# Performance work log

Hardware: AMD Instinct MI355X
Metric: run time of the kernel (lower is better)

Reference implementation:

```python
import jax, jax.numpy as jnp
import numpy as np

N, C, K = 200000, 128, 27  # active voxels, channels, 3x3x3 kernel taps
EPS = 1e-5  # torch LayerNorm default


def setup_inputs() -> dict:
    key = jax.random.key(0)
    ks = jax.random.split(key, 8)
    feats = jax.random.normal(ks[0], (N, C), dtype=jnp.float32)
    # plan-based gather map: neighbor row index per voxel per kernel tap
    neighbor_idx = jax.random.randint(ks[1], (N, K), 0, N, dtype=jnp.int32)
    # sparse conv weights: one [C_in, C_out] slice per kernel offset
    conv_w = jax.random.normal(ks[2], (K, C, C), dtype=jnp.float32) * (1.0 / np.sqrt(K * C))
    conv_b = jax.random.normal(ks[3], (C,), dtype=jnp.float32) * 0.02
    # torch.nn.Linear(C, C): weight [out, in], y = x @ W^T + b
    lin_w = jax.random.normal(ks[4], (C, C), dtype=jnp.float32) * (1.0 / np.sqrt(C))
    lin_b = jax.random.normal(ks[5], (C,), dtype=jnp.float32) * 0.02
    ln_w = 1.0 + 0.02 * jax.random.normal(ks[6], (C,), dtype=jnp.float32)
    ln_b = 0.02 * jax.random.normal(ks[7], (C,), dtype=jnp.float32)
    return {
        "feats": feats, "neighbor_idx": neighbor_idx,
        "conv_w": conv_w, "conv_b": conv_b,
        "lin_w": lin_w, "lin_b": lin_b,
        "ln_w": ln_w, "ln_b": ln_b,
    }


def _sparse_conv(feats, neighbor_idx, conv_w, conv_b):
    # Stream over the 27 kernel taps: gather [N,C] then GEMM with the tap's
    # [C,C] slice; never materialize the [N,27,C] gathered tensor.
    def step(acc, tap):
        idx_k, w_k = tap  # idx_k: [N], w_k: [C, C]
        return acc + feats[idx_k] @ w_k, None

    acc0 = jnp.zeros((feats.shape[0], conv_w.shape[2]), dtype=feats.dtype)
    out, _ = jax.lax.scan(step, acc0, (neighbor_idx.T, conv_w))
    return out + conv_b


def reference(feats, neighbor_idx, conv_w, conv_b, lin_w, lin_b, ln_w, ln_b):
    x = _sparse_conv(feats, neighbor_idx, conv_w, conv_b)   # [N, C]
    x = x @ lin_w.T + lin_b                                  # Linear
    mu = jnp.mean(x, axis=-1, keepdims=True)                 # LayerNorm
    var = jnp.mean(jnp.square(x - mu), axis=-1, keepdims=True)
    x = (x - mu) * jax.lax.rsqrt(var + EPS) * ln_w + ln_b
    return x
```

## Files before the change

### kernel.cpp

```cpp
#include <hip/hip_runtime.h>
#include <hip/hip_bf16.h>
#include <stdint.h>

#define N_ROWS 200000
#define C_DIM  128
#define TAPS   27
#define EPS    1e-5f

typedef __attribute__((ext_vector_type(8)))  short  short8;
typedef __attribute__((ext_vector_type(16))) float  floatx16;

__device__ __forceinline__ unsigned int f2bf(float f) {
  union { float f; unsigned int u; } v; v.f = f;
  unsigned int r = v.u + 0x7FFFu + ((v.u >> 16) & 1u);
  return r >> 16;
}

__device__ __forceinline__ void glds16(const unsigned short* g, unsigned short* l) {
  __builtin_amdgcn_global_load_lds(
      (const __attribute__((address_space(1))) unsigned int*)g,
      (__attribute__((address_space(3))) unsigned int*)l, 16, 0, 0);
}

__global__ __launch_bounds__(256) void k_cast(const float* __restrict__ in,
                                              unsigned short* __restrict__ out, int n8) {
  int i = blockIdx.x * 256 + threadIdx.x;
  if (i >= n8) return;
  const float4* p = (const float4*)in + (size_t)i * 2;
  float4 a = p[0], b = p[1];
  uint4 v;
  v.x = f2bf(a.x) | (f2bf(a.y) << 16);
  v.y = f2bf(a.z) | (f2bf(a.w) << 16);
  v.z = f2bf(b.x) | (f2bf(b.y) << 16);
  v.w = f2bf(b.z) | (f2bf(b.w) << 16);
  *(uint4*)(out + (size_t)i * 8) = v;
}

__global__ __launch_bounds__(256) void k_fold(const float* __restrict__ conv_w,
                                              const float* __restrict__ lin_w,
                                              const float* __restrict__ conv_b,
                                              const float* __restrict__ lin_b,
                                              unsigned short* __restrict__ wfrag,
                                              float* __restrict__ biasf) {
  __shared__ float lwT[128 * 128];
  for (int e = threadIdx.x; e < 16384; e += 256) {
    int co = e >> 7, t = e & 127;
    lwT[t * 128 + (co ^ (t & 31))] = lin_w[e];
  }
  __syncthreads();

  int id = blockIdx.x * 256 + threadIdx.x;
  const int NW = TAPS * 4 * 8 * 64;
  if (id < NW) {
    int l  = id & 63;
    int s  = (id >> 6) & 7;
    int nt = (id >> 9) & 3;
    int k  = id >> 11;
    int ci0 = s * 16 + (l >> 5) * 8;
    int co  = nt * 32 + (l & 31);
    const float* cw = conv_w + ((size_t)(k * 128 + ci0)) * 128;
    float acc[8] = {0, 0, 0, 0, 0, 0, 0, 0};
    for (int t = 0; t < 128; ++t) {
      float lv = lwT[t * 128 + (co ^ (t & 31))];
#pragma unroll
      for (int j = 0; j < 8; ++j) acc[j] += cw[j * 128 + t] * lv;
    }
    uint4 v;
    v.x = f2bf(acc[0]) | (f2bf(acc[1]) << 16);
    v.y = f2bf(acc[2]) | (f2bf(acc[3]) << 16);
    v.z = f2bf(acc[4]) | (f2bf(acc[5]) << 16);
    v.w = f2bf(acc[6]) | (f2bf(acc[7]) << 16);
    *(uint4*)(wfrag + (size_t)id * 8) = v;
  } else if (id < NW + 128) {
    int co = id - NW;
    float s = lin_b[co];
    for (int t = 0; t < 128; ++t) s += conv_b[t] * lwT[t * 128 + (co ^ (t & 31))];
    biasf[co] = s;
  }
}

__global__ __launch_bounds__(512, 4) void k_main(const unsigned short* __restrict__ featsB,
                                                 const int* __restrict__ nidx,
                                                 const unsigned short* __restrict__ wfrag,
                                                 const float* __restrict__ biasf,
                                                 const float* __restrict__ lnw,
                                                 const float* __restrict__ lnb,
                                                 float* __restrict__ out) {
  __shared__ unsigned short ldsB[2][16384];

  const int tid = threadIdx.x;
  const int l   = tid & 63;
  const int w   = tid >> 6;
  const int l31 = l & 31;
  const int lh  = l >> 5;
  const int row0w = blockIdx.x * 256 + w * 32;
  const int gr  = row0w + l31;
  const int grc = (gr < N_ROWS) ? gr : 0;
  const int* np = nidx + (size_t)grc * TAPS;

  floatx16 acc0 = {0.f}, acc1 = {0.f}, acc2 = {0.f}, acc3 = {0.f};

  {
    const unsigned short* src = wfrag + (size_t)tid * 8;
    unsigned short* dst = &ldsB[0][w * 512];
#pragma unroll
    for (int r = 0; r < 4; ++r) glds16(src + r * 4096, dst + r * 4096);
  }
  int nid = np[0];

  for (int k = 0; k < TAPS; ++k) {
    const int cur = k & 1;
    if (k + 1 < TAPS) {
      const unsigned short* src = wfrag + (size_t)(k + 1) * 16384 + (size_t)tid * 8;
      unsigned short* dst = &ldsB[cur ^ 1][w * 512];
#pragma unroll
      for (int r = 0; r < 4; ++r) glds16(src + r * 4096, dst + r * 4096);
      __builtin_amdgcn_s_waitcnt(0xF74);
    } else {
      __builtin_amdgcn_s_waitcnt(0xF70);
    }
    __builtin_amdgcn_s_barrier();

    const short8* ap = (const short8*)(featsB + (size_t)(unsigned)nid * 128 + lh * 8);
    short8 a0 = ap[0],  a1 = ap[2],  a2 = ap[4],  a3 = ap[6];
    short8 a4 = ap[8],  a5 = ap[10], a6 = ap[12], a7 = ap[14];
    int nid_next = (k + 1 < TAPS) ? np[k + 1] : 0;

    const unsigned short* bb = &ldsB[cur][l * 8];
#pragma unroll
    for (int s = 0; s < 8; ++s) {
      short8 av = (s == 0) ? a0 : (s == 1) ? a1 : (s == 2) ? a2 : (s == 3) ? a3
                : (s == 4) ? a4 : (s == 5) ? a5 : (s == 6) ? a6 : a7;
      short8 b0 = *(const short8*)(bb + (0 * 8 + s) * 512);
      short8 b1 = *(const short8*)(bb + (1 * 8 + s) * 512);
      short8 b2 = *(const short8*)(bb + (2 * 8 + s) * 512);
      short8 b3 = *(const short8*)(bb + (3 * 8 + s) * 512);
      acc0 = __builtin_amdgcn_mfma_f32_32x32x16_bf16(av, b0, acc0, 0, 0, 0);
      acc1 = __builtin_amdgcn_mfma_f32_32x32x16_bf16(av, b1, acc1, 0, 0, 0);
      acc2 = __builtin_amdgcn_mfma_f32_32x32x16_bf16(av, b2, acc2, 0, 0, 0);
      acc3 = __builtin_amdgcn_mfma_f32_32x32x16_bf16(av, b3, acc3, 0, 0, 0);
    }
    __builtin_amdgcn_s_barrier();
    nid = nid_next;
  }

  float b0 = biasf[l31], b1 = biasf[32 + l31], b2 = biasf[64 + l31], b3 = biasf[96 + l31];
  float g0 = lnw[l31],   g1 = lnw[32 + l31],   g2 = lnw[64 + l31],   g3 = lnw[96 + l31];
  float c0 = lnb[l31],   c1 = lnb[32 + l31],   c2 = lnb[64 + l31],   c3 = lnb[96 + l31];

#pragma unroll
  for (int r = 0; r < 16; ++r) {
    float x0 = acc0[r] + b0, x1 = acc1[r] + b1, x2 = acc2[r] + b2, x3 = acc3[r] + b3;
    float s = x0 + x1 + x2 + x3;
    float q = x0 * x0 + x1 * x1 + x2 * x2 + x3 * x3;
#pragma unroll
    for (int off = 16; off >= 1; off >>= 1) {
      s += __shfl_xor(s, off, 64);
      q += __shfl_xor(q, off, 64);
    }
    float mu  = s * (1.0f / 128.0f);
    float var = q * (1.0f / 128.0f) - mu * mu;
    float rs  = rsqrtf(var + EPS);
    int row   = (r & 3) + 8 * (r >> 2) + 4 * lh;
    int grow  = row0w + row;
    if (grow < N_ROWS) {
      float* o = out + (size_t)grow * 128;
      o[l31]      = (x0 - mu) * rs * g0 + c0;
      o[32 + l31] = (x1 - mu) * rs * g1 + c1;
      o[64 + l31] = (x2 - mu) * rs * g2 + c2;
      o[96 + l31] = (x3 - mu) * rs * g3 + c3;
    }
  }
}

extern "C" void kernel_launch(void* const* d_in, const int* in_sizes, int n_in,
                              void* d_out, int out_size, void* d_ws, size_t ws_size,
                              hipStream_t stream) {
  const float* feats  = (const float*)d_in[0];
  const int*   nidx   = (const int*)d_in[1];
  const float* conv_w = (const float*)d_in[2];
  const float* conv_b = (const float*)d_in[3];
  const float* lin_w  = (const float*)d_in[4];
  const float* lin_b  = (const float*)d_in[5];
  const float* ln_w   = (const float*)d_in[6];
  const float* ln_b   = (const float*)d_in[7];
  float* out = (float*)d_out;

  unsigned short* featsB = (unsigned short*)d_ws;
  unsigned short* wfrag  = (unsigned short*)((char*)d_ws + 51200000);
  float*          biasf  = (float*)((char*)d_ws + 51200000 + 884736);

  int n8 = N_ROWS * C_DIM / 8;
  k_cast<<<(n8 + 255) / 256, 256, 0, stream>>>(feats, featsB, n8);
  k_fold<<<(TAPS * 2048 + 128 + 255) / 256, 256, 0, stream>>>(conv_w, lin_w, conv_b, lin_b,
                                                              wfrag, biasf);
  k_main<<<(N_ROWS + 255) / 256, 512, 0, stream>>>(featsB, nidx, wfrag, biasf, ln_w, ln_b, out);
}
```

Measured before the change: 507.4 us.

## Software-pipeline neighbor feature gathers one tap ahead of MFMA compute

Restructures the tap loop so each lane's bf16 feature row for tap k+1 is loaded right after that slice has been consumed by the MFMAs for tap k. The neighbor index is likewise fetched two taps ahead, and the last tap is peeled into a separate epilogue. The aim is to hide the random-gather latency behind matrix-core work instead of stalling at the top of every iteration. In exchange it adds sched_barrier fences and a hand-tuned waitcnt that must correctly order the global-to-LDS weight copies against the extra outstanding gathers, and it raises pressure on a tight register budget.

```diff
diff --git a/kernel.cpp b/kernel.cpp
--- a/kernel.cpp
+++ b/kernel.cpp
@@ -79,6 +79,32 @@
   }
 }
 
+
+#define STEP_LD(s, av)                                                       \
+  {                                                                          \
+    short8 b0 = *(const short8*)(bb + (0 * 8 + s) * 512);                    \
+    short8 b1 = *(const short8*)(bb + (1 * 8 + s) * 512);                    \
+    short8 b2 = *(const short8*)(bb + (2 * 8 + s) * 512);                    \
+    short8 b3 = *(const short8*)(bb + (3 * 8 + s) * 512);                    \
+    acc0 = __builtin_amdgcn_mfma_f32_32x32x16_bf16(av, b0, acc0, 0, 0, 0);   \
+    acc1 = __builtin_amdgcn_mfma_f32_32x32x16_bf16(av, b1, acc1, 0, 0, 0);   \
+    acc2 = __builtin_amdgcn_mfma_f32_32x32x16_bf16(av, b2, acc2, 0, 0, 0);   \
+    acc3 = __builtin_amdgcn_mfma_f32_32x32x16_bf16(av, b3, acc3, 0, 0, 0);   \
+    av = apn[s * 2];                                                         \
+  }
+
+#define STEP_NL(s, av)                                                       \
+  {                                                                          \
+    short8 b0 = *(const short8*)(bb + (0 * 8 + s) * 512);                    \
+    short8 b1 = *(const short8*)(bb + (1 * 8 + s) * 512);                    \
+    short8 b2 = *(const short8*)(bb + (2 * 8 + s) * 512);                    \
+    short8 b3 = *(const short8*)(bb + (3 * 8 + s) * 512);                    \
+    acc0 = __builtin_amdgcn_mfma_f32_32x32x16_bf16(av, b0, acc0, 0, 0, 0);   \
+    acc1 = __builtin_amdgcn_mfma_f32_32x32x16_bf16(av, b1, acc1, 0, 0, 0);   \
+    acc2 = __builtin_amdgcn_mfma_f32_32x32x16_bf16(av, b2, acc2, 0, 0, 0);   \
+    acc3 = __builtin_amdgcn_mfma_f32_32x32x16_bf16(av, b3, acc3, 0, 0, 0);   \
+  }
+
 __global__ __launch_bounds__(512, 4) void k_main(const unsigned short* __restrict__ featsB,
                                                  const int* __restrict__ nidx,
                                                  const unsigned short* __restrict__ wfrag,
@@ -100,48 +126,53 @@
 
   floatx16 acc0 = {0.f}, acc1 = {0.f}, acc2 = {0.f}, acc3 = {0.f};
 
+  int nid0 = np[0];
+  int nidB = np[1];
+
   {
     const unsigned short* src = wfrag + (size_t)tid * 8;
     unsigned short* dst = &ldsB[0][w * 512];
 #pragma unroll
     for (int r = 0; r < 4; ++r) glds16(src + r * 4096, dst + r * 4096);
   }
-  int nid = np[0];
-
-  for (int k = 0; k < TAPS; ++k) {
+
+  short8 a0, a1, a2, a3, a4, a5, a6, a7;
+  {
+    const short8* ap = (const short8*)(featsB + (size_t)(unsigned)nid0 * 128 + lh * 8);
+    a0 = ap[0];  a1 = ap[2];  a2 = ap[4];  a3 = ap[6];
+    a4 = ap[8];  a5 = ap[10]; a6 = ap[12]; a7 = ap[14];
+  }
+
+  for (int k = 0; k < TAPS - 1; ++k) {
     const int cur = k & 1;
-    if (k + 1 < TAPS) {
+    {
       const unsigned short* src = wfrag + (size_t)(k + 1) * 16384 + (size_t)tid * 8;
       unsigned short* dst = &ldsB[cur ^ 1][w * 512];
 #pragma unroll
       for (int r = 0; r < 4; ++r) glds16(src + r * 4096, dst + r * 4096);
-      __builtin_amdgcn_s_waitcnt(0xF74);
-    } else {
-      __builtin_amdgcn_s_waitcnt(0xF70);
-    }
+    }
+    __builtin_amdgcn_sched_barrier(0);
+    __builtin_amdgcn_s_waitcnt(0xF78);
     __builtin_amdgcn_s_barrier();
 
-    const short8* ap = (const short8*)(featsB + (size_t)(unsigned)nid * 128 + lh * 8);
-    short8 a0 = ap[0],  a1 = ap[2],  a2 = ap[4],  a3 = ap[6];
-    short8 a4 = ap[8],  a5 = ap[10], a6 = ap[12], a7 = ap[14];
-    int nid_next = (k + 1 < TAPS) ? np[k + 1] : 0;
-
+    int nidC = np[(k + 2 < TAPS) ? (k + 2) : (TAPS - 1)];
+    const short8* apn = (const short8*)(featsB + (size_t)(unsigned)nidB * 128 + lh * 8);
     const unsigned short* bb = &ldsB[cur][l * 8];
-#pragma unroll
-    for (int s = 0; s < 8; ++s) {
-      short8 av = (s == 0) ? a0 : (s == 1) ? a1 : (s == 2) ? a2 : (s == 3) ? a3
-                : (s == 4) ? a4 : (s == 5) ? a5 : (s == 6) ? a6 : a7;
-      short8 b0 = *(const short8*)(bb + (0 * 8 + s) * 512);
-      short8 b1 = *(const short8*)(bb + (1 * 8 + s) * 512);
-      short8 b2 = *(const short8*)(bb + (2 * 8 + s) * 512);
-      short8 b3 = *(const short8*)(bb + (3 * 8 + s) * 512);
-      acc0 = __builtin_amdgcn_mfma_f32_32x32x16_bf16(av, b0, acc0, 0, 0, 0);
-      acc1 = __builtin_amdgcn_mfma_f32_32x32x16_bf16(av, b1, acc1, 0, 0, 0);
-      acc2 = __builtin_amdgcn_mfma_f32_32x32x16_bf16(av, b2, acc2, 0, 0, 0);
-      acc3 = __builtin_amdgcn_mfma_f32_32x32x16_bf16(av, b3, acc3, 0, 0, 0);
-    }
+
+    STEP_LD(0, a0) STEP_LD(1, a1) STEP_LD(2, a2) STEP_LD(3, a3)
+    STEP_LD(4, a4) STEP_LD(5, a5) STEP_LD(6, a6) STEP_LD(7, a7)
+
+    __builtin_amdgcn_sched_barrier(0);
     __builtin_amdgcn_s_barrier();
-    nid = nid_next;
+    nidB = nidC;
+  }
+
+  {
+    __builtin_amdgcn_s_waitcnt(0xF78);
+    __builtin_amdgcn_s_barrier();
+    const unsigned short* bb = &ldsB[(TAPS - 1) & 1][l * 8];
+    STEP_NL(0, a0) STEP_NL(1, a1) STEP_NL(2, a2) STEP_NL(3, a3)
+    STEP_NL(4, a4) STEP_NL(5, a5) STEP_NL(6, a6) STEP_NL(7, a7)
   }
 
   float b0 = biasf[l31], b1 = biasf[32 + l31], b2 = biasf[64 + l31], b3 = biasf[96 + l31];
```

New measurement: 518.9 us. +2.3%, slower.

## Transpose neighbor index table and gather features via buffer loads with cache policy

Applied to the files above, without the earlier changes.

Adds a transpose kernel that turns the [N,27] neighbor index table into tap-major [27,N] when the workspace is large enough, so each tap's per-row index loads coalesce across the wave. The feature gathers in the main kernel are switched to raw buffer loads with a cache-policy bit set, aiming to change how the random row gathers sit in cache. This costs an extra pass that reads and writes the index table, plus a workspace-size check that picks the path at runtime.

```diff
diff --git a/kernel.cpp b/kernel.cpp
--- a/kernel.cpp
+++ b/kernel.cpp
@@ -10,6 +10,12 @@
 typedef __attribute__((ext_vector_type(8)))  short  short8;
 typedef __attribute__((ext_vector_type(16))) float  floatx16;
 
+#if __has_builtin(__builtin_amdgcn_make_buffer_rsrc) && __has_builtin(__builtin_amdgcn_raw_buffer_load_b128)
+#define GATHER_SC0 1
+#else
+#define GATHER_SC0 0
+#endif
+
 __device__ __forceinline__ unsigned int f2bf(float f) {
   union { float f; unsigned int u; } v; v.f = f;
   unsigned int r = v.u + 0x7FFFu + ((v.u >> 16) & 1u);
@@ -21,6 +27,13 @@
       (const __attribute__((address_space(1))) unsigned int*)g,
       (__attribute__((address_space(3))) unsigned int*)l, 16, 0, 0);
 }
+
+#if GATHER_SC0
+__device__ __forceinline__ short8 ld16sc0(__amdgpu_buffer_rsrc_t r, int voff) {
+  return __builtin_bit_cast(short8,
+      __builtin_amdgcn_raw_buffer_load_b128(r, voff, 0, 1));
+}
+#endif
 
 __global__ __launch_bounds__(256) void k_cast(const float* __restrict__ in,
                                               unsigned short* __restrict__ out, int n8) {
@@ -34,6 +47,20 @@
   v.z = f2bf(b.x) | (f2bf(b.y) << 16);
   v.w = f2bf(b.z) | (f2bf(b.w) << 16);
   *(uint4*)(out + (size_t)i * 8) = v;
+}
+
+__global__ __launch_bounds__(256) void k_tr(const int* __restrict__ in,
+                                            int* __restrict__ outT) {
+  __shared__ int t[1728];
+  const int tile = blockIdx.x;
+  const int* src = in + (size_t)tile * 1728;
+  for (int e = threadIdx.x; e < 1728; e += 256) t[e] = src[e];
+  __syncthreads();
+  const int base = tile * 64;
+  for (int o = threadIdx.x; o < 1728; o += 256) {
+    int k = o >> 6, r = o & 63;
+    outT[(size_t)k * N_ROWS + base + r] = t[r * 27 + k];
+  }
 }
 
 __global__ __launch_bounds__(256) void k_fold(const float* __restrict__ conv_w,
@@ -80,7 +107,8 @@
 }
 
 __global__ __launch_bounds__(512, 4) void k_main(const unsigned short* __restrict__ featsB,
-                                                 const int* __restrict__ nidx,
+                                                 const int* __restrict__ ntab,
+                                                 const int nrs, const int nts,
                                                  const unsigned short* __restrict__ wfrag,
                                                  const float* __restrict__ biasf,
                                                  const float* __restrict__ lnw,
@@ -96,7 +124,12 @@
   const int row0w = blockIdx.x * 256 + w * 32;
   const int gr  = row0w + l31;
   const int grc = (gr < N_ROWS) ? gr : 0;
-  const int* np = nidx + (size_t)grc * TAPS;
+  const int* np = ntab + (size_t)grc * nrs;
+
+#if GATHER_SC0
+  __amdgpu_buffer_rsrc_t rsrc = __builtin_amdgcn_make_buffer_rsrc(
+      (void*)featsB, (short)0, N_ROWS * C_DIM * 2, 0x00020000);
+#endif
 
   floatx16 acc0 = {0.f}, acc1 = {0.f}, acc2 = {0.f}, acc3 = {0.f};
 
@@ -121,10 +154,22 @@
     }
     __builtin_amdgcn_s_barrier();
 
+#if GATHER_SC0
+    const int voff = ((int)(unsigned)nid << 8) + (lh << 4);
+    short8 a0 = ld16sc0(rsrc, voff);
+    short8 a1 = ld16sc0(rsrc, voff + 32);
+    short8 a2 = ld16sc0(rsrc, voff + 64);
+    short8 a3 = ld16sc0(rsrc, voff + 96);
+    short8 a4 = ld16sc0(rsrc, voff + 128);
+    short8 a5 = ld16sc0(rsrc, voff + 160);
+    short8 a6 = ld16sc0(rsrc, voff + 192);
+    short8 a7 = ld16sc0(rsrc, voff + 224);
+#else
     const short8* ap = (const short8*)(featsB + (size_t)(unsigned)nid * 128 + lh * 8);
     short8 a0 = ap[0],  a1 = ap[2],  a2 = ap[4],  a3 = ap[6];
     short8 a4 = ap[8],  a5 = ap[10], a6 = ap[12], a7 = ap[14];
-    int nid_next = (k + 1 < TAPS) ? np[k + 1] : 0;
+#endif
+    int nid_next = (k + 1 < TAPS) ? np[(k + 1) * nts] : 0;
 
     const unsigned short* bb = &ldsB[cur][l * 8];
 #pragma unroll
@@ -189,10 +234,21 @@
   unsigned short* featsB = (unsigned short*)d_ws;
   unsigned short* wfrag  = (unsigned short*)((char*)d_ws + 51200000);
   float*          biasf  = (float*)((char*)d_ws + 51200000 + 884736);
+  int*            nidxT  = (int*)((char*)d_ws + 51200000 + 884736 + 512);
+
+  const size_t ws_need_tr = 51200000ULL + 884736ULL + 512ULL + 21600000ULL;
+  const bool use_tr = (ws_size >= ws_need_tr);
 
   int n8 = N_ROWS * C_DIM / 8;
   k_cast<<<(n8 + 255) / 256, 256, 0, stream>>>(feats, featsB, n8);
   k_fold<<<(TAPS * 2048 + 128 + 255) / 256, 256, 0, stream>>>(conv_w, lin_w, conv_b, lin_b,
                                                               wfrag, biasf);
-  k_main<<<(N_ROWS + 255) / 256, 512, 0, stream>>>(featsB, nidx, wfrag, biasf, ln_w, ln_b, out);
-}
+  if (use_tr) k_tr<<<N_ROWS / 64, 256, 0, stream>>>(nidx, nidxT);
+
+  k_main<<<(N_ROWS + 255) / 256, 512, 0, stream>>>(
+      featsB,
+      use_tr ? (const int*)nidxT : nidx,
+      use_tr ? 1 : TAPS,
+      use_tr ? N_ROWS : 1,
+      wfrag, biasf, ln_w, ln_b, out);
+}
```

After: 511.7 us. About the same (+0.9%).

## Stage gathered rows into LDS via async loads and pipeline quarter-tap weight tiles

Applied to the files above, without the earlier changes.

The main kernel is restructured into 128-thread blocks of 64 rows. Gathered feature rows now go into swizzled LDS through global_load_lds, with neighbor indices shuffled across lanes using ds_bpermute. Weights are streamed in quarter-tap chunks through a double buffer under explicit waitcnt, barriers and sched_barrier. The weight fragment layout is reordered to match, and an optional transpose kernel writes the neighbor table tap-major when workspace allows, so index loads coalesce. This aims to hide gather latency behind MFMA work, at the cost of an extra launch, more barriers and smaller blocks.

```diff
diff --git a/kernel.cpp b/kernel.cpp
--- a/kernel.cpp
+++ b/kernel.cpp
@@ -9,6 +9,11 @@
 
 typedef __attribute__((ext_vector_type(8)))  short  short8;
 typedef __attribute__((ext_vector_type(16))) float  floatx16;
+
+#define SBAR()  __builtin_amdgcn_s_barrier()
+#define SCHED() __builtin_amdgcn_sched_barrier(0)
+#define WAITV(n) __builtin_amdgcn_s_waitcnt(0xF70 | (n))
+#define LGKM0() asm volatile("s_waitcnt lgkmcnt(0)" ::: "memory")
 
 __device__ __forceinline__ unsigned int f2bf(float f) {
   union { float f; unsigned int u; } v; v.f = f;
@@ -36,6 +41,20 @@
   *(uint4*)(out + (size_t)i * 8) = v;
 }
 
+__global__ __launch_bounds__(256) void k_tr(const int* __restrict__ in,
+                                            int* __restrict__ outT) {
+  __shared__ int t[1728];
+  const int tile = blockIdx.x;
+  const int* src = in + (size_t)tile * 1728;
+  for (int e = threadIdx.x; e < 1728; e += 256) t[e] = src[e];
+  __syncthreads();
+  const int base = tile * 64;
+  for (int o = threadIdx.x; o < 1728; o += 256) {
+    int k = o >> 6, r = o & 63;
+    outT[(size_t)k * N_ROWS + base + r] = t[r * 27 + k];
+  }
+}
+
 __global__ __launch_bounds__(256) void k_fold(const float* __restrict__ conv_w,
                                               const float* __restrict__ lin_w,
                                               const float* __restrict__ conv_b,
@@ -50,12 +69,14 @@
   __syncthreads();
 
   int id = blockIdx.x * 256 + threadIdx.x;
-  const int NW = TAPS * 4 * 8 * 64;
+  const int NW = TAPS * 4 * 4 * 2 * 64;
   if (id < NW) {
     int l  = id & 63;
-    int s  = (id >> 6) & 7;
-    int nt = (id >> 9) & 3;
+    int sh = (id >> 6) & 1;
+    int nt = (id >> 7) & 3;
+    int qr = (id >> 9) & 3;
     int k  = id >> 11;
+    int s  = qr * 2 + sh;
     int ci0 = s * 16 + (l >> 5) * 8;
     int co  = nt * 32 + (l & 31);
     const float* cw = conv_w + ((size_t)(k * 128 + ci0)) * 128;
@@ -79,78 +100,151 @@
   }
 }
 
-__global__ __launch_bounds__(512, 4) void k_main(const unsigned short* __restrict__ featsB,
-                                                 const int* __restrict__ nidx,
+__global__ __launch_bounds__(128, 2) void k_main(const unsigned short* __restrict__ featsB,
+                                                 const int* __restrict__ ntab,
+                                                 const int nrs, const int nts,
                                                  const unsigned short* __restrict__ wfrag,
                                                  const float* __restrict__ biasf,
                                                  const float* __restrict__ lnw,
                                                  const float* __restrict__ lnb,
                                                  float* __restrict__ out) {
-  __shared__ unsigned short ldsB[2][16384];
+  __shared__ unsigned short A_lds[2][4096];
+  __shared__ unsigned short B_lds[2][4096];
 
   const int tid = threadIdx.x;
   const int l   = tid & 63;
   const int w   = tid >> 6;
   const int l31 = l & 31;
   const int lh  = l >> 5;
-  const int row0w = blockIdx.x * 256 + w * 32;
+  const int row0w = blockIdx.x * 64 + w * 32;
   const int gr  = row0w + l31;
   const int grc = (gr < N_ROWS) ? gr : 0;
-  const int* np = nidx + (size_t)grc * TAPS;
+  const int* np = ntab + (size_t)grc * nrs;
+
+  const int q4 = l >> 4;
+  const int cb = (l & 15) ^ q4;
+  const int rx = l31 & 7;
+  unsigned short* Aw = &A_lds[w][0];
+  const unsigned short* Ar = Aw + l31 * 128;
+
+#define ASTAGE(nv) do {                                                      \
+    _Pragma("unroll")                                                        \
+    for (int i_ = 0; i_ < 8; ++i_) {                                         \
+      int nidl = __builtin_amdgcn_ds_bpermute((i_ << 4) + (q4 << 2), (nv));  \
+      int cc = cb ^ ((i_ & 1) << 2);                                         \
+      const unsigned short* s_ =                                             \
+          featsB + ((size_t)(unsigned)nidl << 7) + (cc << 3);                \
+      glds16(s_, Aw + i_ * 512);                                             \
+    }                                                                        \
+  } while (0)
+
+#define AREAD() do {                                                         \
+    a0 = *(const short8*)(Ar + (((0  + lh) ^ rx) << 3));                     \
+    a1 = *(const short8*)(Ar + (((2  + lh) ^ rx) << 3));                     \
+    a2 = *(const short8*)(Ar + (((4  + lh) ^ rx) << 3));                     \
+    a3 = *(const short8*)(Ar + (((6  + lh) ^ rx) << 3));                     \
+    a4 = *(const short8*)(Ar + (((8  + lh) ^ rx) << 3));                     \
+    a5 = *(const short8*)(Ar + (((10 + lh) ^ rx) << 3));                     \
+    a6 = *(const short8*)(Ar + (((12 + lh) ^ rx) << 3));                     \
+    a7 = *(const short8*)(Ar + (((14 + lh) ^ rx) << 3));                     \
+  } while (0)
+
+#define BSTAGE(Qi, slot) do {                                                \
+    int Qc = (Qi) > 4 * TAPS - 1 ? 4 * TAPS - 1 : (Qi);                      \
+    const unsigned short* s_ = wfrag + (size_t)Qc * 4096 + w * 2048 + l * 8; \
+    unsigned short* d_ = &B_lds[slot][w * 2048];                             \
+    glds16(s_, d_);                                                          \
+    glds16(s_ + 512, d_ + 512);                                              \
+    glds16(s_ + 1024, d_ + 1024);                                            \
+    glds16(s_ + 1536, d_ + 1536);                                            \
+  } while (0)
+
+#define BREAD8(slot) do {                                                    \
+    const unsigned short* bb = &B_lds[slot][l * 8];                          \
+    b0 = *(const short8*)(bb + 0 * 512);                                     \
+    b1 = *(const short8*)(bb + 1 * 512);                                     \
+    b2 = *(const short8*)(bb + 2 * 512);                                     \
+    b3 = *(const short8*)(bb + 3 * 512);                                     \
+    b4 = *(const short8*)(bb + 4 * 512);                                     \
+    b5 = *(const short8*)(bb + 5 * 512);                                     \
+    b6 = *(const short8*)(bb + 6 * 512);                                     \
+    b7 = *(const short8*)(bb + 7 * 512);                                     \
+  } while (0)
+
+#define MFMA8(aA, aB) do {                                                   \
+    acc0 = __builtin_amdgcn_mfma_f32_32x32x16_bf16(aA, b0, acc0, 0, 0, 0);   \
+    acc1 = __builtin_amdgcn_mfma_f32_32x32x16_bf16(aA, b2, acc1, 0, 0, 0);   \
+    acc2 = __builtin_amdgcn_mfma_f32_32x32x16_bf16(aA, b4, acc2, 0, 0, 0);   \
+    acc3 = __builtin_amdgcn_mfma_f32_32x32x16_bf16(aA, b6, acc3, 0, 0, 0);   \
+    acc0 = __builtin_amdgcn_mfma_f32_32x32x16_bf16(aB, b1, acc0, 0, 0, 0);   \
+    acc1 = __builtin_amdgcn_mfma_f32_32x32x16_bf16(aB, b3, acc1, 0, 0, 0);   \
+    acc2 = __builtin_amdgcn_mfma_f32_32x32x16_bf16(aB, b5, acc2, 0, 0, 0);   \
+    acc3 = __builtin_amdgcn_mfma_f32_32x32x16_bf16(aB, b7, acc3, 0, 0, 0);   \
+  } while (0)
 
   floatx16 acc0 = {0.f}, acc1 = {0.f}, acc2 = {0.f}, acc3 = {0.f};
-
-  {
-    const unsigned short* src = wfrag + (size_t)tid * 8;
-    unsigned short* dst = &ldsB[0][w * 512];
-#pragma unroll
-    for (int r = 0; r < 4; ++r) glds16(src + r * 4096, dst + r * 4096);
-  }
-  int nid = np[0];
-
-  for (int k = 0; k < TAPS; ++k) {
-    const int cur = k & 1;
-    if (k + 1 < TAPS) {
-      const unsigned short* src = wfrag + (size_t)(k + 1) * 16384 + (size_t)tid * 8;
-      unsigned short* dst = &ldsB[cur ^ 1][w * 512];
-#pragma unroll
-      for (int r = 0; r < 4; ++r) glds16(src + r * 4096, dst + r * 4096);
-      __builtin_amdgcn_s_waitcnt(0xF74);
-    } else {
-      __builtin_amdgcn_s_waitcnt(0xF70);
+  short8 a0, a1, a2, a3, a4, a5, a6, a7;
+  short8 b0, b1, b2, b3, b4, b5, b6, b7;
+
+  int nid0 = np[0];
+  int n_stage = np[nts];
+  int n_next;
+  WAITV(0);
+  SCHED();
+  ASTAGE(nid0);
+  BSTAGE(0, 0);
+  BSTAGE(1, 1);
+  SCHED();
+
+  for (int t = 0; t < TAPS; ++t) {
+    WAITV(4);
+    AREAD();
+    SCHED(); SBAR(); SCHED();
+    BREAD8(0);
+    LGKM0(); SCHED(); SBAR(); SCHED();
+    {
+      const int tf = (t + 2 < TAPS) ? (t + 2) : (TAPS - 1);
+      n_next = np[(size_t)tf * nts];
     }
-    __builtin_amdgcn_s_barrier();
-
-    const short8* ap = (const short8*)(featsB + (size_t)(unsigned)nid * 128 + lh * 8);
-    short8 a0 = ap[0],  a1 = ap[2],  a2 = ap[4],  a3 = ap[6];
-    short8 a4 = ap[8],  a5 = ap[10], a6 = ap[12], a7 = ap[14];
-    int nid_next = (k + 1 < TAPS) ? np[k + 1] : 0;
-
-    const unsigned short* bb = &ldsB[cur][l * 8];
-#pragma unroll
-    for (int s = 0; s < 8; ++s) {
-      short8 av = (s == 0) ? a0 : (s == 1) ? a1 : (s == 2) ? a2 : (s == 3) ? a3
-                : (s == 4) ? a4 : (s == 5) ? a5 : (s == 6) ? a6 : a7;
-      short8 b0 = *(const short8*)(bb + (0 * 8 + s) * 512);
-      short8 b1 = *(const short8*)(bb + (1 * 8 + s) * 512);
-      short8 b2 = *(const short8*)(bb + (2 * 8 + s) * 512);
-      short8 b3 = *(const short8*)(bb + (3 * 8 + s) * 512);
-      acc0 = __builtin_amdgcn_mfma_f32_32x32x16_bf16(av, b0, acc0, 0, 0, 0);
-      acc1 = __builtin_amdgcn_mfma_f32_32x32x16_bf16(av, b1, acc1, 0, 0, 0);
-      acc2 = __builtin_amdgcn_mfma_f32_32x32x16_bf16(av, b2, acc2, 0, 0, 0);
-      acc3 = __builtin_amdgcn_mfma_f32_32x32x16_bf16(av, b3, acc3, 0, 0, 0);
-    }
-    __builtin_amdgcn_s_barrier();
-    nid = nid_next;
-  }
-
-  float b0 = biasf[l31], b1 = biasf[32 + l31], b2 = biasf[64 + l31], b3 = biasf[96 + l31];
+    BSTAGE(4 * t + 2, 0);
+    SCHED();
+    MFMA8(a0, a1);
+
+    WAITV(5);
+    SCHED(); SBAR(); SCHED();
+    BREAD8(1);
+    LGKM0(); SCHED(); SBAR(); SCHED();
+    BSTAGE(4 * t + 3, 1);
+    SCHED();
+    MFMA8(a2, a3);
+
+    WAITV(4);
+    SCHED(); SBAR(); SCHED();
+    BREAD8(0);
+    LGKM0(); SCHED(); SBAR(); SCHED();
+    ASTAGE(n_stage);
+    BSTAGE(4 * t + 4, 0);
+    SCHED();
+    MFMA8(a4, a5);
+
+    WAITV(12);
+    SCHED(); SBAR(); SCHED();
+    BREAD8(1);
+    LGKM0(); SCHED(); SBAR(); SCHED();
+    BSTAGE(4 * t + 5, 1);
+    SCHED();
+    MFMA8(a6, a7);
+
+    n_stage = n_next;
+  }
+
+  float e0 = biasf[l31], e1 = biasf[32 + l31], e2 = biasf[64 + l31], e3 = biasf[96 + l31];
   float g0 = lnw[l31],   g1 = lnw[32 + l31],   g2 = lnw[64 + l31],   g3 = lnw[96 + l31];
   float c0 = lnb[l31],   c1 = lnb[32 + l31],   c2 = lnb[64 + l31],   c3 = lnb[96 + l31];
 
 #pragma unroll
   for (int r = 0; r < 16; ++r) {
-    float x0 = acc0[r] + b0, x1 = acc1[r] + b1, x2 = acc2[r] + b2, x3 = acc3[r] + b3;
+    float x0 = acc0[r] + e0, x1 = acc1[r] + e1, x2 = acc2[r] + e2, x3 = acc3[r] + e3;
     float s = x0 + x1 + x2 + x3;
     float q = x0 * x0 + x1 * x1 + x2 * x2 + x3 * x3;
 #pragma unroll
@@ -189,10 +283,21 @@
   unsigned short* featsB = (unsigned short*)d_ws;
   unsigned short* wfrag  = (unsigned short*)((char*)d_ws + 51200000);
   float*          biasf  = (float*)((char*)d_ws + 51200000 + 884736);
+  int*            nidxT  = (int*)((char*)d_ws + 51200000 + 884736 + 512);
+
+  const size_t ws_need_tr = 51200000ULL + 884736ULL + 512ULL + 21600000ULL;
+  const bool use_tr = (ws_size >= ws_need_tr);
 
   int n8 = N_ROWS * C_DIM / 8;
   k_cast<<<(n8 + 255) / 256, 256, 0, stream>>>(feats, featsB, n8);
   k_fold<<<(TAPS * 2048 + 128 + 255) / 256, 256, 0, stream>>>(conv_w, lin_w, conv_b, lin_b,
                                                               wfrag, biasf);
-  k_main<<<(N_ROWS + 255) / 256, 512, 0, stream>>>(featsB, nidx, wfrag, biasf, ln_w, ln_b, out);
-}
+  if (use_tr) k_tr<<<N_ROWS / 64, 256, 0, stream>>>(nidx, nidxT);
+
+  k_main<<<(N_ROWS + 63) / 64, 128, 0, stream>>>(
+      featsB,
+      use_tr ? (const int*)nidxT : nidx,
+      use_tr ? 1 : TAPS,
+      use_tr ? N_ROWS : 1,
+      wfrag, biasf, ln_w, ln_b, out);
+}
```

New measurement: 524.2 us. 1.03x slower.
